# Kernel optimization log

Hardware: AMD Instinct MI355X
Metric: run time of the kernel (lower is better)

The kernel has to match this reference:

```python
import jax, jax.numpy as jnp
import numpy as np

EPS = 1e-05
POOL = 10  # pooling_kernel

def setup_inputs() -> dict:
    key = jax.random.key(0)
    x = jax.random.normal(key, (8, 16, 2000, 128), dtype=jnp.float32)
    return {"x": x}

def reference(x) -> jnp.ndarray:
    B, C, T, F = x.shape
    # (B, C, T, F) -> (B, C*F, T), matching permute(0,1,3,2).reshape
    xr = jnp.transpose(x, (0, 1, 3, 2)).reshape(B, C * F, T)
    T1 = T // POOL
    # pooled block means of x and x^2 (AvgPool1d kernel=stride=POOL)
    blocks = xr[:, :, : T1 * POOL].reshape(B, C * F, T1, POOL)
    pm = blocks.mean(-1)            # (B, CF, T1)
    pm2 = (blocks ** 2).mean(-1)    # (B, CF, T1)
    # causal cumulative mean over pooled blocks (replaces O(T1^2) mask-multiply)
    nfrms = jnp.arange(1, T1 + 1, dtype=xr.dtype)  # (T1,)
    cmean = jnp.cumsum(pm, axis=-1) / nfrms
    cmean2 = jnp.cumsum(pm2, axis=-1) / nfrms
    var = cmean2 - cmean ** 2
    # repeat each block stat POOL times along time
    mean_t = jnp.repeat(cmean, POOL, axis=-1)  # (B, CF, T1*POOL)
    var_t = jnp.repeat(var, POOL, axis=-1)
    if T1 * POOL < T:  # pad tail with last stat (static branch)
        pad = T - T1 * POOL
        mean_t = jnp.concatenate([mean_t, jnp.repeat(mean_t[:, :, -1:], pad, axis=-1)], axis=-1)
        var_t = jnp.concatenate([var_t, jnp.repeat(var_t[:, :, -1:], pad, axis=-1)], axis=-1)
    x_norm = (xr - mean_t) / jnp.sqrt(var_t + EPS)
    # (B, CF, T) -> (B, C, F, T) -> (B, C, T, F)
    return jnp.transpose(x_norm.reshape(B, C, F, T), (0, 1, 3, 2))
```

## Files before the change

kernel.cpp:

```cpp
#include <hip/hip_runtime.h>

#define B_    8
#define C_    16
#define T_    2000
#define F_    128
#define POOL_ 10
#define T1_   200
#define BC_   (B_*C_)
#define EPS_  1e-5f

__global__ __launch_bounds__(256) void k1_blocksums(
    const float4* __restrict__ x4, float4* __restrict__ S4, float4* __restrict__ S24)
{
    int bid = blockIdx.x;
    int bc  = bid / (T1_ / 8);
    int t1  = (bid % (T1_ / 8)) * 8 + (threadIdx.x >> 5);
    int f4  = threadIdx.x & 31;

    const float4* p = x4 + (size_t)(bc * T_ + t1 * POOL_) * (F_ / 4) + f4;
    float4 s  = {0.f, 0.f, 0.f, 0.f};
    float4 s2 = {0.f, 0.f, 0.f, 0.f};
#pragma unroll
    for (int k = 0; k < POOL_; ++k) {
        float4 v = p[(size_t)k * (F_ / 4)];
        s.x += v.x; s.y += v.y; s.z += v.z; s.w += v.w;
        s2.x = fmaf(v.x, v.x, s2.x);
        s2.y = fmaf(v.y, v.y, s2.y);
        s2.z = fmaf(v.z, v.z, s2.z);
        s2.w = fmaf(v.w, v.w, s2.w);
    }
    size_t o = (size_t)(bc * T1_ + t1) * (F_ / 4) + f4;
    S4[o]  = s;
    S24[o] = s2;
}

__global__ __launch_bounds__(64) void k2_scan(
    float* __restrict__ S, float* __restrict__ S2)
{
    int g  = blockIdx.x * 64 + threadIdx.x;
    int bc = g / F_;
    int f  = g - bc * F_;

    float rs = 0.f, rs2 = 0.f;
    size_t idx = (size_t)bc * T1_ * F_ + f;
#pragma unroll 4
    for (int t1 = 0; t1 < T1_; ++t1, idx += F_) {
        rs  += S[idx];
        rs2 += S2[idx];
        float inv = 1.0f / (float)((t1 + 1) * POOL_);
        float m   = rs  * inv;
        float m2  = rs2 * inv;
        float var = m2 - m * m;
        S[idx]  = m;
        S2[idx] = rsqrtf(var + EPS_);
    }
}

__global__ __launch_bounds__(256) void k3_norm(
    const float4* __restrict__ x4, const float4* __restrict__ M4,
    const float4* __restrict__ R4, float4* __restrict__ out4)
{
    int gid = blockIdx.x * 256 + threadIdx.x;
    int f4  = gid & (F_ / 4 - 1);
    int tmp = gid >> 5;
    int t   = tmp % T_;
    int bc  = tmp / T_;

    size_t sidx = (size_t)(bc * T1_ + t / POOL_) * (F_ / 4) + f4;
    float4 xv = x4[gid];
    float4 m  = M4[sidx];
    float4 r  = R4[sidx];
    float4 o;
    o.x = (xv.x - m.x) * r.x;
    o.y = (xv.y - m.y) * r.y;
    o.z = (xv.z - m.z) * r.z;
    o.w = (xv.w - m.w) * r.w;
    out4[gid] = o;
}

extern "C" void kernel_launch(void* const* d_in, const int* in_sizes, int n_in,
                              void* d_out, int out_size, void* d_ws, size_t ws_size,
                              hipStream_t stream)
{
    const float* x   = (const float*)d_in[0];
    float*       out = (float*)d_out;

    float* S  = (float*)d_ws;
    float* S2 = S + (size_t)BC_ * T1_ * F_;

    k1_blocksums<<<BC_ * (T1_ / 8), 256, 0, stream>>>(
        (const float4*)x, (float4*)S, (float4*)S2);

    k2_scan<<<BC_ * F_ / 64, 64, 0, stream>>>(S, S2);

    k3_norm<<<(BC_ * T_ * (F_ / 4)) / 256, 256, 0, stream>>>(
        (const float4*)x, (const float4*)S, (const float4*)S2, (float4*)out);
}
```

Before: 271.6 us.

## Fuse block sums, causal scan and normalization into one streaming kernel

Replaces the three-kernel pipeline (block sums, per-feature scan, normalize) with one kernel. Each workgroup streams one (b,c) feature half through time in chunks of 8 pooled blocks, and keeps the running sums in shared memory. Each chunk's values stay in registers for the normalize step, with the next chunk prefetched into registers. This cuts a second full read of x and the workspace round-trips. In exchange the grid shrinks to 256 workgroups that walk time serially with two barriers per chunk, which risks low occupancy and latency-bound streaming.

Measured after the change: 229.8 us. 15.4% less time.

```diff
diff --git a/kernel.cpp b/kernel.cpp
--- a/kernel.cpp
+++ b/kernel.cpp
@@ -4,95 +4,129 @@
 #define C_    16
 #define T_    2000
 #define F_    128
+#define F4_   32
 #define POOL_ 10
 #define T1_   200
-#define BC_   (B_*C_)
+#define BC_   128
 #define EPS_  1e-5f
 
-__global__ __launch_bounds__(256) void k1_blocksums(
-    const float4* __restrict__ x4, float4* __restrict__ S4, float4* __restrict__ S24)
+#define G_      8
+#define NCHUNK_ 25
+#define HF4_    16
+
+__global__ __launch_bounds__(256) void fused_cumnorm(
+    const float4* __restrict__ x4, float4* __restrict__ out4)
 {
-    int bid = blockIdx.x;
-    int bc  = bid / (T1_ / 8);
-    int t1  = (bid % (T1_ / 8)) * 8 + (threadIdx.x >> 5);
-    int f4  = threadIdx.x & 31;
+    const int tid  = (int)threadIdx.x;
+    const int bc   = (int)blockIdx.x >> 1;
+    const int half = (int)blockIdx.x & 1;
+    const int g    = tid >> 5;
+    const int k2   = (tid >> 4) & 1;
+    const int f4   = tid & 15;
 
-    const float4* p = x4 + (size_t)(bc * T_ + t1 * POOL_) * (F_ / 4) + f4;
-    float4 s  = {0.f, 0.f, 0.f, 0.f};
-    float4 s2 = {0.f, 0.f, 0.f, 0.f};
+    __shared__ float4 sS  [G_][HF4_];
+    __shared__ float4 sS2 [G_][HF4_];
+    __shared__ float4 runS [2][HF4_];
+    __shared__ float4 runS2[2][HF4_];
+
+    const size_t tbase = (size_t)bc * T_ * F4_ + (size_t)half * HF4_ + (size_t)f4
+                       + (size_t)(g * POOL_ + k2) * F4_;
+    const float4* __restrict__ pc = x4   + tbase;
+    float4*       __restrict__ qc = out4 + tbase;
+
+    const int RS = 2 * F4_;
+    const int CS = G_ * POOL_ * F4_;
+
+    float4 v0 = pc[0], v1 = pc[RS], v2 = pc[2*RS], v3 = pc[3*RS], v4 = pc[4*RS];
+
+    if (tid < HF4_) {
+        runS [0][tid] = make_float4(0.f, 0.f, 0.f, 0.f);
+        runS2[0][tid] = make_float4(0.f, 0.f, 0.f, 0.f);
+    }
+
+    for (int c = 0; c < NCHUNK_; ++c) {
+        float4 s, s2;
+        s.x = ((v0.x + v1.x) + (v2.x + v3.x)) + v4.x;
+        s.y = ((v0.y + v1.y) + (v2.y + v3.y)) + v4.y;
+        s.z = ((v0.z + v1.z) + (v2.z + v3.z)) + v4.z;
+        s.w = ((v0.w + v1.w) + (v2.w + v3.w)) + v4.w;
+        s2.x = v0.x*v0.x; s2.x = fmaf(v1.x,v1.x,s2.x); s2.x = fmaf(v2.x,v2.x,s2.x); s2.x = fmaf(v3.x,v3.x,s2.x); s2.x = fmaf(v4.x,v4.x,s2.x);
+        s2.y = v0.y*v0.y; s2.y = fmaf(v1.y,v1.y,s2.y); s2.y = fmaf(v2.y,v2.y,s2.y); s2.y = fmaf(v3.y,v3.y,s2.y); s2.y = fmaf(v4.y,v4.y,s2.y);
+        s2.z = v0.z*v0.z; s2.z = fmaf(v1.z,v1.z,s2.z); s2.z = fmaf(v2.z,v2.z,s2.z); s2.z = fmaf(v3.z,v3.z,s2.z); s2.z = fmaf(v4.z,v4.z,s2.z);
+        s2.w = v0.w*v0.w; s2.w = fmaf(v1.w,v1.w,s2.w); s2.w = fmaf(v2.w,v2.w,s2.w); s2.w = fmaf(v3.w,v3.w,s2.w); s2.w = fmaf(v4.w,v4.w,s2.w);
+
+        s.x  += __shfl_xor(s.x , 16);
+        s.y  += __shfl_xor(s.y , 16);
+        s.z  += __shfl_xor(s.z , 16);
+        s.w  += __shfl_xor(s.w , 16);
+        s2.x += __shfl_xor(s2.x, 16);
+        s2.y += __shfl_xor(s2.y, 16);
+        s2.z += __shfl_xor(s2.z, 16);
+        s2.w += __shfl_xor(s2.w, 16);
+
+        float4 w0, w1, w2, w3, w4;
+        if (c + 1 < NCHUNK_) {
+            const float4* pn = pc + CS;
+            w0 = pn[0]; w1 = pn[RS]; w2 = pn[2*RS]; w3 = pn[3*RS]; w4 = pn[4*RS];
+        } else {
+            w0 = v0; w1 = v1; w2 = v2; w3 = v3; w4 = v4;
+        }
+
+        if (k2 == 0) { sS[g][f4] = s; sS2[g][f4] = s2; }
+        __syncthreads();
+
+        float4 acc  = runS [c & 1][f4];
+        float4 acc2 = runS2[c & 1][f4];
 #pragma unroll
-    for (int k = 0; k < POOL_; ++k) {
-        float4 v = p[(size_t)k * (F_ / 4)];
-        s.x += v.x; s.y += v.y; s.z += v.z; s.w += v.w;
-        s2.x = fmaf(v.x, v.x, s2.x);
-        s2.y = fmaf(v.y, v.y, s2.y);
-        s2.z = fmaf(v.z, v.z, s2.z);
-        s2.w = fmaf(v.w, v.w, s2.w);
+        for (int j = 0; j < G_; ++j) {
+            float4 aj  = sS [j][f4];
+            float4 a2j = sS2[j][f4];
+            if (j <= g) {
+                acc.x  += aj.x;  acc.y  += aj.y;  acc.z  += aj.z;  acc.w  += aj.w;
+                acc2.x += a2j.x; acc2.y += a2j.y; acc2.z += a2j.z; acc2.w += a2j.w;
+            }
+        }
+
+        const float inv = 1.0f / (float)((c * G_ + g + 1) * POOL_);
+        float4 mean, rstd;
+        mean.x = acc.x * inv; rstd.x = rsqrtf(fmaf(-mean.x, mean.x, acc2.x * inv) + EPS_);
+        mean.y = acc.y * inv; rstd.y = rsqrtf(fmaf(-mean.y, mean.y, acc2.y * inv) + EPS_);
+        mean.z = acc.z * inv; rstd.z = rsqrtf(fmaf(-mean.z, mean.z, acc2.z * inv) + EPS_);
+        mean.w = acc.w * inv; rstd.w = rsqrtf(fmaf(-mean.w, mean.w, acc2.w * inv) + EPS_);
+
+        float4 o;
+        o.x = (v0.x - mean.x) * rstd.x; o.y = (v0.y - mean.y) * rstd.y;
+        o.z = (v0.z - mean.z) * rstd.z; o.w = (v0.w - mean.w) * rstd.w;
+        qc[0] = o;
+        o.x = (v1.x - mean.x) * rstd.x; o.y = (v1.y - mean.y) * rstd.y;
+        o.z = (v1.z - mean.z) * rstd.z; o.w = (v1.w - mean.w) * rstd.w;
+        qc[RS] = o;
+        o.x = (v2.x - mean.x) * rstd.x; o.y = (v2.y - mean.y) * rstd.y;
+        o.z = (v2.z - mean.z) * rstd.z; o.w = (v2.w - mean.w) * rstd.w;
+        qc[2*RS] = o;
+        o.x = (v3.x - mean.x) * rstd.x; o.y = (v3.y - mean.y) * rstd.y;
+        o.z = (v3.z - mean.z) * rstd.z; o.w = (v3.w - mean.w) * rstd.w;
+        qc[3*RS] = o;
+        o.x = (v4.x - mean.x) * rstd.x; o.y = (v4.y - mean.y) * rstd.y;
+        o.z = (v4.z - mean.z) * rstd.z; o.w = (v4.w - mean.w) * rstd.w;
+        qc[4*RS] = o;
+
+        if (g == G_ - 1 && k2 == 0) {
+            runS [(c + 1) & 1][f4] = acc;
+            runS2[(c + 1) & 1][f4] = acc2;
+        }
+        __syncthreads();
+
+        v0 = w0; v1 = w1; v2 = w2; v3 = w3; v4 = w4;
+        pc += CS; qc += CS;
     }
-    size_t o = (size_t)(bc * T1_ + t1) * (F_ / 4) + f4;
-    S4[o]  = s;
-    S24[o] = s2;
-}
-
-__global__ __launch_bounds__(64) void k2_scan(
-    float* __restrict__ S, float* __restrict__ S2)
-{
-    int g  = blockIdx.x * 64 + threadIdx.x;
-    int bc = g / F_;
-    int f  = g - bc * F_;
-
-    float rs = 0.f, rs2 = 0.f;
-    size_t idx = (size_t)bc * T1_ * F_ + f;
-#pragma unroll 4
-    for (int t1 = 0; t1 < T1_; ++t1, idx += F_) {
-        rs  += S[idx];
-        rs2 += S2[idx];
-        float inv = 1.0f / (float)((t1 + 1) * POOL_);
-        float m   = rs  * inv;
-        float m2  = rs2 * inv;
-        float var = m2 - m * m;
-        S[idx]  = m;
-        S2[idx] = rsqrtf(var + EPS_);
-    }
-}
-
-__global__ __launch_bounds__(256) void k3_norm(
-    const float4* __restrict__ x4, const float4* __restrict__ M4,
-    const float4* __restrict__ R4, float4* __restrict__ out4)
-{
-    int gid = blockIdx.x * 256 + threadIdx.x;
-    int f4  = gid & (F_ / 4 - 1);
-    int tmp = gid >> 5;
-    int t   = tmp % T_;
-    int bc  = tmp / T_;
-
-    size_t sidx = (size_t)(bc * T1_ + t / POOL_) * (F_ / 4) + f4;
-    float4 xv = x4[gid];
-    float4 m  = M4[sidx];
-    float4 r  = R4[sidx];
-    float4 o;
-    o.x = (xv.x - m.x) * r.x;
-    o.y = (xv.y - m.y) * r.y;
-    o.z = (xv.z - m.z) * r.z;
-    o.w = (xv.w - m.w) * r.w;
-    out4[gid] = o;
 }
 
 extern "C" void kernel_launch(void* const* d_in, const int* in_sizes, int n_in,
                               void* d_out, int out_size, void* d_ws, size_t ws_size,
                               hipStream_t stream)
 {
-    const float* x   = (const float*)d_in[0];
-    float*       out = (float*)d_out;
-
-    float* S  = (float*)d_ws;
-    float* S2 = S + (size_t)BC_ * T1_ * F_;
-
-    k1_blocksums<<<BC_ * (T1_ / 8), 256, 0, stream>>>(
-        (const float4*)x, (float4*)S, (float4*)S2);
-
-    k2_scan<<<BC_ * F_ / 64, 64, 0, stream>>>(S, S2);
-
-    k3_norm<<<(BC_ * T_ * (F_ / 4)) / 256, 256, 0, stream>>>(
-        (const float4*)x, (const float4*)S, (const float4*)S2, (float4*)out);
+    (void)in_sizes; (void)n_in; (void)d_ws; (void)ws_size; (void)out_size;
+    fused_cumnorm<<<BC_ * 2, 256, 0, stream>>>(
+        (const float4*)d_in[0], (float4*)d_out);
 }
```

## Fuse block sums, causal scan and normalization into one wave-per-slice kernel

Applied to the files above, without the earlier changes.

Replaces the three-kernel pipeline (block sums, serial scan, normalize) with a single kernel in which each 64-lane wave owns one (bc, quarter of F) slice. It walks time in groups of four pooled blocks, reducing within each group and scanning across it with shuffles, while prefetching registers two groups ahead. Each x element is read once and normalized right away, with no workspace round trips and no second read of x. The cost is only 512 single-wave blocks, each running a long serial dependency chain, so occupancy and latency hiding are limited.

After: 236.9 us. 1.15x faster.

```diff
diff --git a/kernel.cpp b/kernel.cpp
--- a/kernel.cpp
+++ b/kernel.cpp
@@ -4,95 +4,123 @@
 #define C_    16
 #define T_    2000
 #define F_    128
+#define F4_   32
 #define POOL_ 10
 #define T1_   200
-#define BC_   (B_*C_)
+#define BC_   128
 #define EPS_  1e-5f
 
-__global__ __launch_bounds__(256) void k1_blocksums(
-    const float4* __restrict__ x4, float4* __restrict__ S4, float4* __restrict__ S24)
+#define NG_   50
+#define GS_   (40 * F4_)
+#define RSR_  (2 * F4_)
+
+
+#define PFX(av)                                                               \
+    { float t1_ = __shfl((av), lm16); (av) += jge1 ? t1_ : 0.0f;              \
+      float t2_ = __shfl((av), lm32); (av) += jge2 ? t2_ : 0.0f; }
+
+#define STEP(kk, V0,V1,V2,V3,V4, P0,P1,P2,P3,P4)                              \
+  {                                                                           \
+        \
+    int kpf_ = (kk) + 2; if (kpf_ >= NG_) kpf_ = 0;                           \
+    const float4* pp_ = pbase + (size_t)kpf_ * GS_;                           \
+    P0 = pp_[0]; P1 = pp_[RSR_]; P2 = pp_[2*RSR_];                            \
+    P3 = pp_[3*RSR_]; P4 = pp_[4*RSR_];                                       \
+              \
+    float4 s_, s2_;                                                           \
+    s_.x = ((V0.x+V1.x)+(V2.x+V3.x))+V4.x;                                    \
+    s_.y = ((V0.y+V1.y)+(V2.y+V3.y))+V4.y;                                    \
+    s_.z = ((V0.z+V1.z)+(V2.z+V3.z))+V4.z;                                    \
+    s_.w = ((V0.w+V1.w)+(V2.w+V3.w))+V4.w;                                    \
+    s2_.x = V0.x*V0.x; s2_.x = fmaf(V1.x,V1.x,s2_.x); s2_.x = fmaf(V2.x,V2.x,s2_.x); s2_.x = fmaf(V3.x,V3.x,s2_.x); s2_.x = fmaf(V4.x,V4.x,s2_.x); \
+    s2_.y = V0.y*V0.y; s2_.y = fmaf(V1.y,V1.y,s2_.y); s2_.y = fmaf(V2.y,V2.y,s2_.y); s2_.y = fmaf(V3.y,V3.y,s2_.y); s2_.y = fmaf(V4.y,V4.y,s2_.y); \
+    s2_.z = V0.z*V0.z; s2_.z = fmaf(V1.z,V1.z,s2_.z); s2_.z = fmaf(V2.z,V2.z,s2_.z); s2_.z = fmaf(V3.z,V3.z,s2_.z); s2_.z = fmaf(V4.z,V4.z,s2_.z); \
+    s2_.w = V0.w*V0.w; s2_.w = fmaf(V1.w,V1.w,s2_.w); s2_.w = fmaf(V2.w,V2.w,s2_.w); s2_.w = fmaf(V3.w,V3.w,s2_.w); s2_.w = fmaf(V4.w,V4.w,s2_.w); \
+            \
+    s_.x  += __shfl_xor(s_.x , 8); s_.y  += __shfl_xor(s_.y , 8);             \
+    s_.z  += __shfl_xor(s_.z , 8); s_.w  += __shfl_xor(s_.w , 8);             \
+    s2_.x += __shfl_xor(s2_.x, 8); s2_.y += __shfl_xor(s2_.y, 8);             \
+    s2_.z += __shfl_xor(s2_.z, 8); s2_.w += __shfl_xor(s2_.w, 8);             \
+                                        \
+    float4 a_ = s_, a2_ = s2_;                                                \
+    PFX(a_.x); PFX(a_.y); PFX(a_.z); PFX(a_.w);                               \
+    PFX(a2_.x); PFX(a2_.y); PFX(a2_.z); PFX(a2_.w);                           \
+      \
+    float4 ct_, ct2_;                                                         \
+    ct_.x  = rs.x  + a_.x;  ct_.y  = rs.y  + a_.y;                            \
+    ct_.z  = rs.z  + a_.z;  ct_.w  = rs.w  + a_.w;                            \
+    ct2_.x = rs2.x + a2_.x; ct2_.y = rs2.y + a2_.y;                           \
+    ct2_.z = rs2.z + a2_.z; ct2_.w = rs2.w + a2_.w;                           \
+    rs.x  += __shfl(a_.x,  lbc); rs.y  += __shfl(a_.y,  lbc);                 \
+    rs.z  += __shfl(a_.z,  lbc); rs.w  += __shfl(a_.w,  lbc);                 \
+    rs2.x += __shfl(a2_.x, lbc); rs2.y += __shfl(a2_.y, lbc);                 \
+    rs2.z += __shfl(a2_.z, lbc); rs2.w += __shfl(a2_.w, lbc);                 \
+                                      \
+    const float inv_ = 1.0f / (float)((((kk) << 2) + j + 1) * POOL_);         \
+    float4 mean_, rstd_;                                                      \
+    mean_.x = ct_.x * inv_; rstd_.x = rsqrtf(fmaf(-mean_.x, mean_.x, ct2_.x * inv_) + EPS_); \
+    mean_.y = ct_.y * inv_; rstd_.y = rsqrtf(fmaf(-mean_.y, mean_.y, ct2_.y * inv_) + EPS_); \
+    mean_.z = ct_.z * inv_; rstd_.z = rsqrtf(fmaf(-mean_.z, mean_.z, ct2_.z * inv_) + EPS_); \
+    mean_.w = ct_.w * inv_; rstd_.w = rsqrtf(fmaf(-mean_.w, mean_.w, ct2_.w * inv_) + EPS_); \
+                                         \
+    float4* qq_ = qbase + (size_t)(kk) * GS_;                                 \
+    float4 o_;                                                                \
+    o_.x=(V0.x-mean_.x)*rstd_.x; o_.y=(V0.y-mean_.y)*rstd_.y;                 \
+    o_.z=(V0.z-mean_.z)*rstd_.z; o_.w=(V0.w-mean_.w)*rstd_.w; qq_[0]      = o_; \
+    o_.x=(V1.x-mean_.x)*rstd_.x; o_.y=(V1.y-mean_.y)*rstd_.y;                 \
+    o_.z=(V1.z-mean_.z)*rstd_.z; o_.w=(V1.w-mean_.w)*rstd_.w; qq_[RSR_]   = o_; \
+    o_.x=(V2.x-mean_.x)*rstd_.x; o_.y=(V2.y-mean_.y)*rstd_.y;                 \
+    o_.z=(V2.z-mean_.z)*rstd_.z; o_.w=(V2.w-mean_.w)*rstd_.w; qq_[2*RSR_] = o_; \
+    o_.x=(V3.x-mean_.x)*rstd_.x; o_.y=(V3.y-mean_.y)*rstd_.y;                 \
+    o_.z=(V3.z-mean_.z)*rstd_.z; o_.w=(V3.w-mean_.w)*rstd_.w; qq_[3*RSR_] = o_; \
+    o_.x=(V4.x-mean_.x)*rstd_.x; o_.y=(V4.y-mean_.y)*rstd_.y;                 \
+    o_.z=(V4.z-mean_.z)*rstd_.z; o_.w=(V4.w-mean_.w)*rstd_.w; qq_[4*RSR_] = o_; \
+  }
+
+__global__ __launch_bounds__(64) void fused_cumnorm_wave(
+    const float4* __restrict__ x4, float4* __restrict__ out4)
 {
-    int bid = blockIdx.x;
-    int bc  = bid / (T1_ / 8);
-    int t1  = (bid % (T1_ / 8)) * 8 + (threadIdx.x >> 5);
-    int f4  = threadIdx.x & 31;
+    const int lane = (int)threadIdx.x;
+    const int bc   = (int)blockIdx.x >> 2;
+    const int q    = (int)blockIdx.x & 3;
+    const int f4   = lane & 7;
+    const int h    = (lane >> 3) & 1;
+    const int j    = lane >> 4;
 
-    const float4* p = x4 + (size_t)(bc * T_ + t1 * POOL_) * (F_ / 4) + f4;
-    float4 s  = {0.f, 0.f, 0.f, 0.f};
-    float4 s2 = {0.f, 0.f, 0.f, 0.f};
-#pragma unroll
-    for (int k = 0; k < POOL_; ++k) {
-        float4 v = p[(size_t)k * (F_ / 4)];
-        s.x += v.x; s.y += v.y; s.z += v.z; s.w += v.w;
-        s2.x = fmaf(v.x, v.x, s2.x);
-        s2.y = fmaf(v.y, v.y, s2.y);
-        s2.z = fmaf(v.z, v.z, s2.z);
-        s2.w = fmaf(v.w, v.w, s2.w);
+    const int  lm16 = (lane - 16) & 63;
+    const int  lm32 = (lane - 32) & 63;
+    const int  lbc  = 48 | (lane & 15);
+    const bool jge1 = (j >= 1), jge2 = (j >= 2);
+
+    const size_t base = (size_t)bc * (T_ * F4_)
+                      + (size_t)(j * POOL_ + h) * F4_
+                      + (size_t)(q * 8 + f4);
+    const float4* __restrict__ pbase = x4   + base;
+    float4*       __restrict__ qbase = out4 + base;
+
+    float4 rs  = {0.f, 0.f, 0.f, 0.f};
+    float4 rs2 = {0.f, 0.f, 0.f, 0.f};
+
+    float4 A0,A1,A2,A3,A4, B0,B1,B2,B3,B4, C0,C1,C2,C3,C4;
+    { const float4* p = pbase;       A0=p[0]; A1=p[RSR_]; A2=p[2*RSR_]; A3=p[3*RSR_]; A4=p[4*RSR_]; }
+    { const float4* p = pbase + GS_; B0=p[0]; B1=p[RSR_]; B2=p[2*RSR_]; B3=p[3*RSR_]; B4=p[4*RSR_]; }
+
+    int k = 0;
+#pragma unroll 1
+    for (int it = 0; it < (NG_ - 2) / 3; ++it) {
+        STEP(k, A0,A1,A2,A3,A4, C0,C1,C2,C3,C4); ++k;
+        STEP(k, B0,B1,B2,B3,B4, A0,A1,A2,A3,A4); ++k;
+        STEP(k, C0,C1,C2,C3,C4, B0,B1,B2,B3,B4); ++k;
     }
-    size_t o = (size_t)(bc * T1_ + t1) * (F_ / 4) + f4;
-    S4[o]  = s;
-    S24[o] = s2;
-}
-
-__global__ __launch_bounds__(64) void k2_scan(
-    float* __restrict__ S, float* __restrict__ S2)
-{
-    int g  = blockIdx.x * 64 + threadIdx.x;
-    int bc = g / F_;
-    int f  = g - bc * F_;
-
-    float rs = 0.f, rs2 = 0.f;
-    size_t idx = (size_t)bc * T1_ * F_ + f;
-#pragma unroll 4
-    for (int t1 = 0; t1 < T1_; ++t1, idx += F_) {
-        rs  += S[idx];
-        rs2 += S2[idx];
-        float inv = 1.0f / (float)((t1 + 1) * POOL_);
-        float m   = rs  * inv;
-        float m2  = rs2 * inv;
-        float var = m2 - m * m;
-        S[idx]  = m;
-        S2[idx] = rsqrtf(var + EPS_);
-    }
-}
-
-__global__ __launch_bounds__(256) void k3_norm(
-    const float4* __restrict__ x4, const float4* __restrict__ M4,
-    const float4* __restrict__ R4, float4* __restrict__ out4)
-{
-    int gid = blockIdx.x * 256 + threadIdx.x;
-    int f4  = gid & (F_ / 4 - 1);
-    int tmp = gid >> 5;
-    int t   = tmp % T_;
-    int bc  = tmp / T_;
-
-    size_t sidx = (size_t)(bc * T1_ + t / POOL_) * (F_ / 4) + f4;
-    float4 xv = x4[gid];
-    float4 m  = M4[sidx];
-    float4 r  = R4[sidx];
-    float4 o;
-    o.x = (xv.x - m.x) * r.x;
-    o.y = (xv.y - m.y) * r.y;
-    o.z = (xv.z - m.z) * r.z;
-    o.w = (xv.w - m.w) * r.w;
-    out4[gid] = o;
+    STEP(k, A0,A1,A2,A3,A4, C0,C1,C2,C3,C4); ++k;
+    STEP(k, B0,B1,B2,B3,B4, A0,A1,A2,A3,A4);
 }
 
 extern "C" void kernel_launch(void* const* d_in, const int* in_sizes, int n_in,
                               void* d_out, int out_size, void* d_ws, size_t ws_size,
                               hipStream_t stream)
 {
-    const float* x   = (const float*)d_in[0];
-    float*       out = (float*)d_out;
-
-    float* S  = (float*)d_ws;
-    float* S2 = S + (size_t)BC_ * T1_ * F_;
-
-    k1_blocksums<<<BC_ * (T1_ / 8), 256, 0, stream>>>(
-        (const float4*)x, (float4*)S, (float4*)S2);
-
-    k2_scan<<<BC_ * F_ / 64, 64, 0, stream>>>(S, S2);
-
-    k3_norm<<<(BC_ * T_ * (F_ / 4)) / 256, 256, 0, stream>>>(
-        (const float4*)x, (const float4*)S, (const float4*)S2, (float4*)out);
+    (void)in_sizes; (void)n_in; (void)d_ws; (void)ws_size; (void)out_size;
+    fused_cumnorm_wave<<<BC_ * 4, 64, 0, stream>>>(
+        (const float4*)d_in[0], (float4*)d_out);
 }
```
